# Kernel tuning notes

Hardware: AMD Instinct MI355X
Metric: run time of the kernel (lower is better)

The kernel has to match this reference:

```python
import jax, jax.numpy as jnp
import numpy as np

B, IN_DIM, N_NODES, N_LEAVES, N_ACTIONS = 131072, 128, 511, 512, 16


def setup_inputs() -> dict:
    key = jax.random.key(0)
    k1, k2, k3, k4 = jax.random.split(key, 4)
    x = jax.random.normal(k1, (B, IN_DIM), dtype=jnp.float32)
    W1 = jax.random.normal(k2, (N_NODES, IN_DIM), dtype=jnp.float32) * 0.1
    b1 = jax.random.normal(k3, (N_NODES,), dtype=jnp.float32) * 0.1
    W2 = jax.random.normal(k4, (N_LEAVES, 2 * N_NODES), dtype=jnp.float32) * 0.05
    # leaf -> action assignment; arange % n_actions guarantees every group non-empty
    leaf_actions = (jnp.arange(N_LEAVES) % N_ACTIONS).astype(jnp.int32)
    return {"x": x, "W1": W1, "b1": b1, "W2": W2, "leaf_actions": leaf_actions}


def reference(x, W1, b1, W2, leaf_actions):
    # linear1
    h = x @ W1.T + b1                      # [B, N_NODES]
    # relu(h) || relu(-h)
    z = jnp.concatenate([jax.nn.relu(h), jax.nn.relu(-h)], axis=1)  # [B, 2*N_NODES]
    # linear2 (no bias)
    y = z @ W2.T                           # [B, N_LEAVES]
    # grouped segment-max over leaf columns, grouped by action id
    pooled = jax.ops.segment_max(y.T, leaf_actions, num_segments=N_ACTIONS).T  # [B, N_ACTIONS]
    return jax.nn.softmax(pooled, axis=-1)
```

## Files before the change

### kernel.cpp

```cpp
#include <hip/hip_runtime.h>
#include <hip/hip_bf16.h>

typedef unsigned short u16;
typedef unsigned int u32;
typedef __attribute__((ext_vector_type(8))) short bf16x8;
typedef __attribute__((ext_vector_type(4))) float f32x4;

#define NROWS   131072
#define KDIM    128
#define NNODES  511
#define NPAD    512
#define NACT    16

__device__ __forceinline__ u16 f2b(float v) {
  return __builtin_bit_cast(u16, __float2bfloat16(v));
}

union Frag {
  bf16x8 v;
  u16    u[8];
  int4   i;
  int    d[4];
};

__device__ __forceinline__ u32 encf(float f) {
  u32 b = __builtin_bit_cast(u32, f);
  return (b & 0x80000000u) ? ~b : (b | 0x80000000u);
}
__device__ __forceinline__ float decf(u32 u) {
  u32 b = (u & 0x80000000u) ? (u & 0x7FFFFFFFu) : ~u;
  return __builtin_bit_cast(float, b);
}

__global__ void prep_k(const float* __restrict__ W1, const float* __restrict__ W2,
                       const float* __restrict__ b1, u16* __restrict__ w1f,
                       u16* __restrict__ wdf, u16* __restrict__ wsf,
                       float* __restrict__ b1p, u32* __restrict__ outi) {
  int bid = blockIdx.x, t = threadIdx.x;
  if (bid < 256) {
    int o = bid * 256 + t;
    int j = o & 7, l = (o >> 3) & 63, kb = (o >> 9) & 3, nt = o >> 11;
    int row = nt * 16 + (l & 15);
    int col = kb * 32 + (l >> 4) * 8 + j;
    w1f[o] = f2b((row < NNODES) ? W1[row * KDIM + col] : 0.f);
  } else if (bid < 2304) {
    int isS = (bid >= 1280);
    int o = (bid - (isS ? 1280 : 256)) * 256 + t;
    int j = o & 7, l = (o >> 3) & 63, kb = (o >> 9) & 15, lt = o >> 13;
    int leaf = lt * 16 + (l & 15);
    int n = kb * 32 + (l >> 4) * 8 + j;
    float va = 0.f, vb = 0.f;
    if (n < NNODES) {
      va = W2[leaf * (2 * NNODES) + n];
      vb = W2[leaf * (2 * NNODES) + NNODES + n];
    }
    float v = isS ? 0.5f * (va + vb) : 0.5f * (va - vb);
    (isS ? wsf : wdf)[o] = f2b(v);
  } else if (bid < 2306) {
    int i = (bid - 2304) * 256 + t;
    if (i < NPAD) b1p[i] = (i < NNODES) ? b1[i] : 0.f;
  } else {
    int i = (bid - 2306) * 256 + t;
    ((uint4*)outi)[i] = make_uint4(0u, 0u, 0u, 0u);
  }
}

__global__ __launch_bounds__(256, 2) void gemm1_k(const float* __restrict__ x,
                                                  const u16* __restrict__ w1f,
                                                  const float* __restrict__ b1p,
                                                  u16* __restrict__ hb) {
  __shared__ u16 xs[4 * 4 * 64 * 8];
  __shared__ u16 hs[4 * 16 * 64 * 8];

  int t = threadIdx.x, wq = t >> 6, l = t & 63;
  int rg = blockIdx.x;
  int lm = l & 15, quad = l >> 4;

  {
    const float4* xg = (const float4*)(x + (size_t)rg * 64 * KDIM);
#pragma unroll
    for (int i = 0; i < 8; ++i) {
      int f = i * 256 + t;
      int row = f >> 5, col = (f & 31) * 4;
      float4 v = xg[f];
      ushort4 b;
      b.x = f2b(v.x); b.y = f2b(v.y); b.z = f2b(v.z); b.w = f2b(v.w);
      int rt = row >> 4, kb = col >> 5;
      int lane = (row & 15) + 16 * ((col >> 3) & 3);
      *(ushort4*)&xs[(((rt * 4 + kb) * 64 + lane) * 8) + (col & 7)] = b;
    }
  }
  __syncthreads();

  f32x4 zero4 = {0.f, 0.f, 0.f, 0.f};
  f32x4 acc[4][8];
#pragma unroll
  for (int rt = 0; rt < 4; ++rt)
#pragma unroll
    for (int ct = 0; ct < 8; ++ct) acc[rt][ct] = zero4;

#pragma unroll 1
  for (int kb = 0; kb < 4; ++kb) {
    Frag a[4];
#pragma unroll
    for (int rt = 0; rt < 4; ++rt)
      a[rt].i = *(const int4*)&xs[((rt * 4 + kb) * 64 + l) * 8];
#pragma unroll
    for (int ct = 0; ct < 8; ++ct) {
      Frag b;
      b.i = *(const int4*)(w1f + (((wq * 8 + ct) * 4 + kb) * 64 + l) * 8);
#pragma unroll
      for (int rt = 0; rt < 4; ++rt)
        acc[rt][ct] = __builtin_amdgcn_mfma_f32_16x16x32_bf16(a[rt].v, b.v, acc[rt][ct], 0, 0, 0);
    }
  }

#pragma unroll
  for (int ct = 0; ct < 8; ++ct) {
    int node = (wq * 8 + ct) * 16 + lm;
    float bias = b1p[node];
    int kb2 = node >> 5;
    int lsub = 16 * ((node >> 3) & 3);
    int j2 = node & 7;
#pragma unroll
    for (int rt = 0; rt < 4; ++rt)
#pragma unroll
      for (int r = 0; r < 4; ++r) {
        int rl = quad * 4 + r;
        hs[((rt * 16 + kb2) * 64 + (rl + lsub)) * 8 + j2] = f2b(acc[rt][ct][r] + bias);
      }
  }
  __syncthreads();

  {
    int4* dst = (int4*)(hb + (size_t)rg * 32768);
    const int4* src = (const int4*)hs;
#pragma unroll
    for (int i = 0; i < 16; ++i) dst[i * 256 + t] = src[i * 256 + t];
  }
}

__global__ __launch_bounds__(512, 4) void gemm2_k(const u16* __restrict__ hb,
                                                  const u16* __restrict__ wdf,
                                                  const u16* __restrict__ wsf,
                                                  u32* __restrict__ pooled) {
  int t = threadIdx.x, w = t >> 6, l = t & 63;
  int bid = blockIdx.x;
  int half = (bid >> 3) & 1;
  int rg = (bid & 7) | ((bid >> 4) << 3);
  int rh = w >> 2, wq = w & 3;
  int lm = l & 15, quad = l >> 4;

  const u16* hbase = hb  + ((size_t)(rg * 8 + rh * 4) * 16) * 512;
  const u16* dbase = wdf + ((size_t)(half * 16 + wq * 4) * 16) * 512;
  const u16* sbase = wsf + ((size_t)(half * 16 + wq * 4) * 16) * 512;

  f32x4 zero4 = {0.f, 0.f, 0.f, 0.f};
  f32x4 acc[4][4];
#pragma unroll
  for (int rt = 0; rt < 4; ++rt)
#pragma unroll
    for (int ct = 0; ct < 4; ++ct) acc[rt][ct] = zero4;

  Frag h4[4], wA[4], wB[4];
#pragma unroll
  for (int rt = 0; rt < 4; ++rt)
    h4[rt].i = *(const int4*)(hbase + ((size_t)rt * 16 + 0) * 512 + l * 8);
#pragma unroll
  for (int ct = 0; ct < 4; ++ct)
    wA[ct].i = *(const int4*)(dbase + ((size_t)ct * 16 + 0) * 512 + l * 8);
#pragma unroll
  for (int ct = 0; ct < 4; ++ct)
    wB[ct].i = *(const int4*)(sbase + ((size_t)ct * 16 + 0) * 512 + l * 8);

#pragma unroll 1
  for (int kb = 0; kb < 16; ++kb) {
    int kn = (kb + 1) & 15;
#pragma unroll
    for (int ct = 0; ct < 4; ++ct)
#pragma unroll
      for (int rt = 0; rt < 4; ++rt)
        acc[rt][ct] = __builtin_amdgcn_mfma_f32_16x16x32_bf16(h4[rt].v, wA[ct].v, acc[rt][ct], 0, 0, 0);
#pragma unroll
    for (int rt = 0; rt < 4; ++rt)
#pragma unroll
      for (int d = 0; d < 4; ++d) h4[rt].d[d] &= 0x7FFF7FFF;
#pragma unroll
    for (int ct = 0; ct < 4; ++ct)
      wA[ct].i = *(const int4*)(dbase + ((size_t)ct * 16 + kn) * 512 + l * 8);
#pragma unroll
    for (int ct = 0; ct < 4; ++ct)
#pragma unroll
      for (int rt = 0; rt < 4; ++rt)
        acc[rt][ct] = __builtin_amdgcn_mfma_f32_16x16x32_bf16(h4[rt].v, wB[ct].v, acc[rt][ct], 0, 0, 0);
#pragma unroll
    for (int ct = 0; ct < 4; ++ct)
      wB[ct].i = *(const int4*)(sbase + ((size_t)ct * 16 + kn) * 512 + l * 8);
#pragma unroll
    for (int rt = 0; rt < 4; ++rt)
      h4[rt].i = *(const int4*)(hbase + ((size_t)rt * 16 + kn) * 512 + l * 8);
  }

#pragma unroll
  for (int rt = 0; rt < 4; ++rt)
#pragma unroll
    for (int r = 0; r < 4; ++r) {
      float mx = acc[rt][0][r];
#pragma unroll
      for (int ct = 1; ct < 4; ++ct) mx = fmaxf(mx, acc[rt][ct][r]);
      int row = rg * 128 + rh * 64 + rt * 16 + quad * 4 + r;
      atomicMax(pooled + row * NACT + lm, encf(mx));
    }
}

__global__ void combine_k(u32* __restrict__ outi) {
  int row = blockIdx.x * 256 + threadIdx.x;
  uint4* p = (uint4*)(outi + (size_t)row * NACT);
  uint4 q[4];
#pragma unroll
  for (int i = 0; i < 4; ++i) q[i] = p[i];
  float v[NACT];
#pragma unroll
  for (int i = 0; i < 4; ++i) {
    v[i * 4 + 0] = decf(q[i].x); v[i * 4 + 1] = decf(q[i].y);
    v[i * 4 + 2] = decf(q[i].z); v[i * 4 + 3] = decf(q[i].w);
  }
  float m = v[0];
#pragma unroll
  for (int a = 1; a < NACT; ++a) m = fmaxf(m, v[a]);
  float s = 0.f;
#pragma unroll
  for (int a = 0; a < NACT; ++a) { float e = __expf(v[a] - m); v[a] = e; s += e; }
  float inv = 1.f / s;
  float4* pf = (float4*)(outi + (size_t)row * NACT);
#pragma unroll
  for (int i = 0; i < 4; ++i) {
    float4 o; o.x = v[i*4+0]*inv; o.y = v[i*4+1]*inv; o.z = v[i*4+2]*inv; o.w = v[i*4+3]*inv;
    pf[i] = o;
  }
}

extern "C" void kernel_launch(void* const* d_in, const int* in_sizes, int n_in,
                              void* d_out, int out_size, void* d_ws, size_t ws_size,
                              hipStream_t stream) {
  const float* x  = (const float*)d_in[0];
  const float* W1 = (const float*)d_in[1];
  const float* b1 = (const float*)d_in[2];
  const float* W2 = (const float*)d_in[3];

  char* ws = (char*)d_ws;
  u16*   hb  = (u16*)ws;
  u16*   w1f = (u16*)(ws + 134217728);
  u16*   wdf = (u16*)(ws + 134217728 + 131072);
  u16*   wsf = (u16*)(ws + 134217728 + 131072 + 524288);
  float* b1p = (float*)(ws + 134217728 + 131072 + 524288 + 524288);

  prep_k   <<<dim3(4354), dim3(256), 0, stream>>>(W1, W2, b1, w1f, wdf, wsf, b1p, (u32*)d_out);
  gemm1_k  <<<dim3(NROWS / 64), dim3(256), 0, stream>>>(x, w1f, b1p, hb);
  gemm2_k  <<<dim3(2048), dim3(512), 0, stream>>>(hb, wdf, wsf, (u32*)d_out);
  combine_k<<<dim3(NROWS / 256), dim3(256), 0, stream>>>((u32*)d_out);
}
```

Before: 277.0 us.

## Stage gemm2 operand tiles through double-buffered LDS with direct global-to-LDS loads

gemm2 used to read the h, Wd and Ws fragments from global memory straight into registers in every wave, so waves sharing the same h rows or weight tiles each fetched them separately. Each block now cooperatively copies the 40 fragment tiles it needs per K step into a double-buffered shared-memory array using global_load_lds, then every wave reads its fragments from LDS. The aim is to cut redundant global/L2 traffic and overlap the next step's loads with the current MFMAs. In exchange it uses about 80 KB of LDS per block, which may limit occupancy below the declared 4 blocks per CU, and it adds a block-wide barrier every K step.

New measurement: 266.2 us. 3.9% less time.

```diff
diff --git a/kernel.cpp b/kernel.cpp
--- a/kernel.cpp
+++ b/kernel.cpp
@@ -144,6 +144,8 @@
                                                   const u16* __restrict__ wdf,
                                                   const u16* __restrict__ wsf,
                                                   u32* __restrict__ pooled) {
+  __shared__ u16 sb[2][40 * 512];
+
   int t = threadIdx.x, w = t >> 6, l = t & 63;
   int bid = blockIdx.x;
   int half = (bid >> 3) & 1;
@@ -151,9 +153,16 @@
   int rh = w >> 2, wq = w & 3;
   int lm = l & 15, quad = l >> 4;
 
-  const u16* hbase = hb  + ((size_t)(rg * 8 + rh * 4) * 16) * 512;
-  const u16* dbase = wdf + ((size_t)(half * 16 + wq * 4) * 16) * 512;
-  const u16* sbase = wsf + ((size_t)(half * 16 + wq * 4) * 16) * 512;
+  const u16* gsrc[5];
+#pragma unroll
+  for (int i = 0; i < 5; ++i) {
+    int f = w * 5 + i;
+    const u16* p;
+    if (f < 8)       p = hb  + ((size_t)(rg * 8 + f) * 16) * 512;
+    else if (f < 24) p = wdf + ((size_t)(half * 16 + (f - 8)) * 16) * 512;
+    else             p = wsf + ((size_t)(half * 16 + (f - 24)) * 16) * 512;
+    gsrc[i] = p + l * 8;
+  }
 
   f32x4 zero4 = {0.f, 0.f, 0.f, 0.f};
   f32x4 acc[4][4];
@@ -162,20 +171,39 @@
 #pragma unroll
     for (int ct = 0; ct < 4; ++ct) acc[rt][ct] = zero4;
 
-  Frag h4[4], wA[4], wB[4];
-#pragma unroll
-  for (int rt = 0; rt < 4; ++rt)
-    h4[rt].i = *(const int4*)(hbase + ((size_t)rt * 16 + 0) * 512 + l * 8);
-#pragma unroll
-  for (int ct = 0; ct < 4; ++ct)
-    wA[ct].i = *(const int4*)(dbase + ((size_t)ct * 16 + 0) * 512 + l * 8);
-#pragma unroll
-  for (int ct = 0; ct < 4; ++ct)
-    wB[ct].i = *(const int4*)(sbase + ((size_t)ct * 16 + 0) * 512 + l * 8);
+#pragma unroll
+  for (int i = 0; i < 5; ++i) {
+    int f = w * 5 + i;
+    __builtin_amdgcn_global_load_lds(
+        (const __attribute__((address_space(1))) void*)(gsrc[i]),
+        (__attribute__((address_space(3))) void*)&sb[0][f * 512], 16, 0, 0);
+  }
+  __syncthreads();
 
 #pragma unroll 1
   for (int kb = 0; kb < 16; ++kb) {
-    int kn = (kb + 1) & 15;
+    int cur = kb & 1;
+    if (kb < 15) {
+#pragma unroll
+      for (int i = 0; i < 5; ++i) {
+        int f = w * 5 + i;
+        __builtin_amdgcn_global_load_lds(
+            (const __attribute__((address_space(1))) void*)(gsrc[i] + (kb + 1) * 512),
+            (__attribute__((address_space(3))) void*)&sb[cur ^ 1][f * 512], 16, 0, 0);
+      }
+    }
+
+    Frag h4[4], wA[4], wB[4];
+#pragma unroll
+    for (int rt = 0; rt < 4; ++rt)
+      h4[rt].i = *(const int4*)&sb[cur][(rh * 4 + rt) * 512 + l * 8];
+#pragma unroll
+    for (int ct = 0; ct < 4; ++ct)
+      wA[ct].i = *(const int4*)&sb[cur][(8 + wq * 4 + ct) * 512 + l * 8];
+#pragma unroll
+    for (int ct = 0; ct < 4; ++ct)
+      wB[ct].i = *(const int4*)&sb[cur][(24 + wq * 4 + ct) * 512 + l * 8];
+
 #pragma unroll
     for (int ct = 0; ct < 4; ++ct)
 #pragma unroll
@@ -187,18 +215,11 @@
       for (int d = 0; d < 4; ++d) h4[rt].d[d] &= 0x7FFF7FFF;
 #pragma unroll
     for (int ct = 0; ct < 4; ++ct)
-      wA[ct].i = *(const int4*)(dbase + ((size_t)ct * 16 + kn) * 512 + l * 8);
-#pragma unroll
-    for (int ct = 0; ct < 4; ++ct)
 #pragma unroll
       for (int rt = 0; rt < 4; ++rt)
         acc[rt][ct] = __builtin_amdgcn_mfma_f32_16x16x32_bf16(h4[rt].v, wB[ct].v, acc[rt][ct], 0, 0, 0);
-#pragma unroll
-    for (int ct = 0; ct < 4; ++ct)
-      wB[ct].i = *(const int4*)(sbase + ((size_t)ct * 16 + kn) * 512 + l * 8);
-#pragma unroll
-    for (int rt = 0; rt < 4; ++rt)
-      h4[rt].i = *(const int4*)(hbase + ((size_t)rt * 16 + kn) * 512 + l * 8);
+
+    __syncthreads();
   }
 
 #pragma unroll
```
